# Performance work log

Measured on AMD Instinct MI355X. Metric: run time of the kernel, lower is better.

The kernel has to match this reference:

```python
import jax, jax.numpy as jnp
import numpy as np

B, S, T = 4, 512, 512
D, F, L, H, V = 512, 2048, 6, 8, 32000
HD = D // H


def setup_inputs() -> dict:
    key = jax.random.key(0)
    ks = list(jax.random.split(key, 16))
    it = iter(ks)

    def w(shape, scale=0.02):
        return jax.random.normal(next(it), shape, jnp.float32) * scale

    enc_in = jax.random.randint(next(it), (B, S), 0, V, dtype=jnp.int32)
    dec_in = jax.random.randint(next(it), (B, T), 0, V, dtype=jnp.int32)

    # sinusoidal positional encoding (make_sine_pos_encoding)
    pos = np.arange(S)[:, None].astype(np.float32)
    i = np.arange(D)[None, :].astype(np.float32)
    angle = pos / np.power(10000.0, (2.0 * np.floor(i / 2.0)) / D)
    pe = np.zeros((S, D), np.float32)
    pe[:, 0::2] = np.sin(angle[:, 0::2])
    pe[:, 1::2] = np.cos(angle[:, 1::2])

    return {
        "enc_in": enc_in,
        "dec_in": dec_in,
        "e_embed": w((V, D)),
        "d_embed": w((V, D)),
        "pos_enc": jnp.asarray(pe),
        "enc_mha_W": w((L, 4, D, D)),      # q,k,v,out
        "enc_mha_b": jnp.zeros((L, 4, D), jnp.float32),
        "enc_ln_g": jnp.ones((L, 2, D), jnp.float32),
        "enc_ln_b": jnp.zeros((L, 2, D), jnp.float32),
        "enc_ffn_W1": w((L, D, F)),
        "enc_ffn_b1": jnp.zeros((L, F), jnp.float32),
        "enc_ffn_W2": w((L, F, D)),
        "enc_ffn_b2": jnp.zeros((L, D), jnp.float32),
        "dec_mha_W": w((L, 8, D, D)),      # self q,k,v,out then cross q,k,v,out
        "dec_mha_b": jnp.zeros((L, 8, D), jnp.float32),
        "dec_ln_g": jnp.ones((L, 3, D), jnp.float32),
        "dec_ln_b": jnp.zeros((L, 3, D), jnp.float32),
        "dec_ffn_W1": w((L, D, F)),
        "dec_ffn_b1": jnp.zeros((L, F), jnp.float32),
        "dec_ffn_W2": w((L, F, D)),
        "dec_ffn_b2": jnp.zeros((L, D), jnp.float32),
    }


def _layer_norm(x, g, b, eps=1e-6):
    m = jnp.mean(x, axis=-1, keepdims=True)
    v = jnp.mean(jnp.square(x - m), axis=-1, keepdims=True)
    return (x - m) * jax.lax.rsqrt(v + eps) * g + b


def _split_heads(x):
    b, n, _ = x.shape
    return x.reshape(b, n, H, HD).transpose(0, 2, 1, 3)  # b h n d


def _mha(xq, xkv, W, b, mask):
    # W: [>=4, D, D] slice of (q,k,v,out); mask: broadcastable to [b,h,nq,nk]
    q = _split_heads(xq @ W[0] + b[0])
    k = _split_heads(xkv @ W[1] + b[1])
    v = _split_heads(xkv @ W[2] + b[2])
    s = jnp.einsum('bhqd,bhkd->bhqk', q, k) / jnp.sqrt(jnp.float32(HD))
    s = s + mask * (-1e9)
    a = jax.nn.softmax(s, axis=-1)
    o = jnp.einsum('bhqk,bhkd->bhqd', a, v)
    o = o.transpose(0, 2, 1, 3).reshape(xq.shape[0], xq.shape[1], D)
    return o @ W[3] + b[3]


def _forward(enc_in, dec_in, e_embed, d_embed, pos_enc,
             enc_mha_W, enc_mha_b, enc_ln_g, enc_ln_b,
             enc_ffn_W1, enc_ffn_b1, enc_ffn_W2, enc_ffn_b2,
             dec_mha_W, dec_mha_b, dec_ln_g, dec_ln_b,
             dec_ffn_W1, dec_ffn_b1, dec_ffn_W2, dec_ffn_b2):
    # masks: 1.0 where attention is blocked
    enc_pad = (enc_in == 0).astype(jnp.float32)[:, None, None, :]   # [B,1,1,S]
    dec_pad = (dec_in == 0).astype(jnp.float32)[:, None, None, :]   # [B,1,1,T]
    la = jnp.triu(jnp.ones((T, T), jnp.float32), k=1)[None, None]   # [1,1,T,T]
    look_ahead = jnp.maximum(la, dec_pad)                           # [B,1,T,T]

    scale = jnp.float32(D) ** 0.5
    e = e_embed[enc_in] * scale + pos_enc[None, :S]
    d = d_embed[dec_in] * scale + pos_enc[None, :T]

    for l in range(L):
        y = _mha(e, e, enc_mha_W[l], enc_mha_b[l], enc_pad)
        e = _layer_norm(e + y, enc_ln_g[l, 0], enc_ln_b[l, 0])
        y = jax.nn.relu(e @ enc_ffn_W1[l] + enc_ffn_b1[l]) @ enc_ffn_W2[l] + enc_ffn_b2[l]
        e = _layer_norm(e + y, enc_ln_g[l, 1], enc_ln_b[l, 1])

    for l in range(L):
        y = _mha(d, d, dec_mha_W[l, 0:4], dec_mha_b[l, 0:4], look_ahead)
        d = _layer_norm(d + y, dec_ln_g[l, 0], dec_ln_b[l, 0])
        y = _mha(d, e, dec_mha_W[l, 4:8], dec_mha_b[l, 4:8], enc_pad)
        d = _layer_norm(d + y, dec_ln_g[l, 1], dec_ln_b[l, 1])
        y = jax.nn.relu(d @ dec_ffn_W1[l] + dec_ffn_b1[l]) @ dec_ffn_W2[l] + dec_ffn_b2[l]
        d = _layer_norm(d + y, dec_ln_g[l, 2], dec_ln_b[l, 2])

    return d @ d_embed.T  # [B,T,V] logits


def reference(enc_in, dec_in, e_embed, d_embed, pos_enc,
              enc_mha_W, enc_mha_b, enc_ln_g, enc_ln_b,
              enc_ffn_W1, enc_ffn_b1, enc_ffn_W2, enc_ffn_b2,
              dec_mha_W, dec_mha_b, dec_ln_g, dec_ln_b,
              dec_ffn_W1, dec_ffn_b1, dec_ffn_W2, dec_ffn_b2):
    return _forward(enc_in, dec_in, e_embed, d_embed, pos_enc,
                    enc_mha_W, enc_mha_b, enc_ln_g, enc_ln_b,
                    enc_ffn_W1, enc_ffn_b1, enc_ffn_W2, enc_ffn_b2,
                    dec_mha_W, dec_mha_b, dec_ln_g, dec_ln_b,
                    dec_ffn_W1, dec_ffn_b1, dec_ffn_W2, dec_ffn_b2)
```

## Files before the change

### kernel.cpp

```cpp
#include <hip/hip_runtime.h>
#include <hip/hip_bf16.h>
#include <math.h>

#define B_ 4
#define S_ 512
#define D_ 512
#define F_ 2048
#define L_ 6
#define H_ 8
#define V_ 32000

typedef unsigned short u16;
typedef __attribute__((ext_vector_type(8))) short bhalf8;
typedef __attribute__((ext_vector_type(4))) float f32x4;

__device__ __forceinline__ u16 f2b(float v) {
    unsigned x = __builtin_bit_cast(unsigned, v);
    return (u16)((x + 0x7FFFu + ((x >> 16) & 1u)) >> 16);
}

#define GLD16(g, l) __builtin_amdgcn_global_load_lds( \
    (const __attribute__((address_space(1))) void*)(g), \
    (__attribute__((address_space(3))) void*)(l), 16, 0, 0)

__device__ __forceinline__ float redmax16(float v) {
    #pragma unroll
    for (int m = 1; m < 16; m <<= 1) v = fmaxf(v, __shfl_xor(v, m));
    return v;
}
__device__ __forceinline__ float redsum16(float v) {
    #pragma unroll
    for (int m = 1; m < 16; m <<= 1) v += __shfl_xor(v, m);
    return v;
}

template<int NWR, int NWC, int WM, int WN, int OUT, int RELU, int MLOOP,
         int SPLITA, int NT, int VTT, int SWZ>
__global__ __launch_bounds__(NWR * NWC * 64)
void mfma_gemm(const u16* __restrict__ A, const u16* __restrict__ A2, int acut,
               const u16* __restrict__ B,
               const float* __restrict__ bias, void* __restrict__ Cv,
               int K, int lda, int ldb, int ldc,
               u16* __restrict__ vtp, int vc0, long zoffC)
{
    constexpr int BM = NWR * WM, BN = NWC * WN;
    constexpr int NW = NWR * NWC;
    constexpr int CH_A = BM / 16, CH_B = BN / 16, CH = CH_A + CH_B;
    constexpr int NI = WM / 16, NJ = WN / 16;
    constexpr int TSTR = BM + 8;

    __shared__ u16 As[2][BM * 32];
    __shared__ u16 Bs[2][BN * 32];
    __shared__ u16 TT[VTT ? 64 * TSTR : 8];

    const int tid = threadIdx.x;
    const int wid = tid >> 6, lane = tid & 63;
    const int wrow = wid / NWC, wcol = wid % NWC;
    long bn, bmbase;
    if (SWZ) {
        long b0 = blockIdx.x;
        long per = (long)gridDim.x >> 3;
        long w = (b0 & 7) * per + (b0 >> 3);
        constexpr int MB = 16 / MLOOP;
        bn = (w / MB) * BN;
        bmbase = w % MB;
    } else {
        bn = (long)blockIdx.x * BN;
        bmbase = (long)blockIdx.y;
    }
    const int r4 = lane >> 2, c4 = lane & 3;
    const int l15 = lane & 15, l4 = lane >> 4;

    const u16* Ause = (SPLITA && bn >= acut) ? A2 : A;
    const long kz = (long)blockIdx.z * K;
    Ause += kz;
    B += kz;

    #pragma unroll 1
    for (int mi = 0; mi < MLOOP; ++mi) {
        const long bm = (bmbase * MLOOP + mi) * BM;

        f32x4 acc[NI][NJ];
        #pragma unroll
        for (int i = 0; i < NI; ++i)
            #pragma unroll
            for (int j = 0; j < NJ; ++j)
                acc[i][j] = (f32x4){0.f, 0.f, 0.f, 0.f};

        #pragma unroll
        for (int t = 0; t < CH / NW; ++t) {
            int c = wid + t * NW;
            if (c < CH_A) {
                GLD16(Ause + (bm + c * 16 + r4) * (long)lda + c4 * 8,
                      &As[0][c * 512 + lane * 8]);
            } else {
                int cb = c - CH_A;
                GLD16(B + (bn + cb * 16 + r4) * (long)ldb + c4 * 8,
                      &Bs[0][cb * 512 + lane * 8]);
            }
        }

        for (int k0 = 0; k0 < K; k0 += 32) {
            const int cur = (k0 >> 5) & 1;
            __syncthreads();
            if (k0 + 32 < K) {
                const int kn = k0 + 32;
                #pragma unroll
                for (int t = 0; t < CH / NW; ++t) {
                    int c = wid + t * NW;
                    if (c < CH_A) {
                        GLD16(Ause + (bm + c * 16 + r4) * (long)lda + kn + c4 * 8,
                              &As[cur ^ 1][c * 512 + lane * 8]);
                    } else {
                        int cb = c - CH_A;
                        GLD16(B + (bn + cb * 16 + r4) * (long)ldb + kn + c4 * 8,
                              &Bs[cur ^ 1][cb * 512 + lane * 8]);
                    }
                }
            }
            bhalf8 af[NI], bfr[NJ];
            #pragma unroll
            for (int i = 0; i < NI; ++i)
                af[i] = *(const bhalf8*)&As[cur][(wrow * WM + i * 16 + l15) * 32 + l4 * 8];
            #pragma unroll
            for (int j = 0; j < NJ; ++j)
                bfr[j] = *(const bhalf8*)&Bs[cur][(wcol * WN + j * 16 + l15) * 32 + l4 * 8];
            #pragma unroll
            for (int i = 0; i < NI; ++i)
                #pragma unroll
                for (int j = 0; j < NJ; ++j)
                    acc[i][j] = __builtin_amdgcn_mfma_f32_16x16x32_bf16(af[i], bfr[j], acc[i][j], 0, 0, 0);
        }

        if (VTT && vtp != nullptr && bn >= vc0) {
            #pragma unroll
            for (int j = 0; j < NJ; ++j) {
                const int cc = wcol * WN + j * 16 + l15;
                const float bv = bias ? bias[bn + cc] : 0.f;
                #pragma unroll
                for (int i = 0; i < NI; ++i) {
                    const int rw = wrow * WM + i * 16 + (l4 << 2);
                    #pragma unroll
                    for (int r = 0; r < 4; ++r)
                        TT[cc * TSTR + rw + r] = f2b(acc[i][j][r] + bv);
                }
            }
            __syncthreads();
            {
                const int cc = tid;
                const u16* src = &TT[cc * TSTR];
                u16* dst = &vtp[(bn - vc0 + cc) * 2048 + bm];
                #pragma unroll
                for (int p = 0; p < BM / 8; ++p)
                    *(uint4*)(dst + p * 8) = *(const uint4*)(src + p * 8);
            }
            __syncthreads();
            continue;
        }

        float* Cf = (float*)Cv + blockIdx.z * zoffC;
        u16*   Cb = (u16*)Cv  + blockIdx.z * zoffC;
        const int rowb = wrow * WM + (l4 << 2);
        const int colb = wcol * WN + l15;
        #pragma unroll
        for (int j = 0; j < NJ; ++j) {
            const long gc = bn + colb + j * 16;
            const float bv = bias ? bias[gc] : 0.f;
            #pragma unroll
            for (int i = 0; i < NI; ++i) {
                const long gr = bm + rowb + i * 16;
                #pragma unroll
                for (int r = 0; r < 4; ++r) {
                    float v = acc[i][j][r] + bv;
                    if (RELU) v = fmaxf(v, 0.f);
                    if (OUT == 0) {
                        if (NT) __builtin_nontemporal_store(v, &Cf[(gr + r) * (long)ldc + gc]);
                        else    Cf[(gr + r) * (long)ldc + gc] = v;
                    } else {
                        Cb[(gr + r) * (long)ldc + gc] = f2b(v);
                    }
                }
            }
        }
    }
}

__global__ __launch_bounds__(512)
void gemm_ln_kernel(const u16* __restrict__ A, const u16* __restrict__ B,
                    const float* __restrict__ bias,
                    float* __restrict__ x, u16* __restrict__ xb,
                    const float* __restrict__ g, const float* __restrict__ bb,
                    int K)
{
    __shared__ u16 As[16 * 32];
    __shared__ u16 Bs[512 * 32];
    __shared__ float red[2][16][8];
    __shared__ float mv[2][16];

    const int tid = threadIdx.x, w = tid >> 6, lane = tid & 63;
    const int l15 = lane & 15, l4 = lane >> 4;
    const int r4 = lane >> 2, c4 = lane & 3;
    const long bm = (long)blockIdx.x * 16;

    f32x4 acc[4];
    #pragma unroll
    for (int j = 0; j < 4; ++j) acc[j] = (f32x4){0.f, 0.f, 0.f, 0.f};

    for (int k0 = 0; k0 < K; k0 += 32) {
        #pragma unroll
        for (int t = 0; t < 5; ++t) {
            int c = w + t * 8;
            if (c < 33) {
                if (c == 0) {
                    GLD16(A + (bm + r4) * (long)K + k0 + c4 * 8, As + lane * 8);
                } else {
                    GLD16(B + ((c - 1) * 16 + r4) * (long)K + k0 + c4 * 8,
                          Bs + (c - 1) * 512 + lane * 8);
                }
            }
        }
        __syncthreads();
        bhalf8 af = *(const bhalf8*)&As[l15 * 32 + l4 * 8];
        #pragma unroll
        for (int j = 0; j < 4; ++j) {
            bhalf8 bf = *(const bhalf8*)&Bs[(w * 64 + j * 16 + l15) * 32 + l4 * 8];
            acc[j] = __builtin_amdgcn_mfma_f32_16x16x32_bf16(af, bf, acc[j], 0, 0, 0);
        }
        __syncthreads();
    }

    float vbuf[4][4], s[4] = {0, 0, 0, 0}, s2[4] = {0, 0, 0, 0};
    #pragma unroll
    for (int j = 0; j < 4; ++j) {
        int col = w * 64 + j * 16 + l15;
        float bv = bias[col];
        #pragma unroll
        for (int r = 0; r < 4; ++r) {
            int row = l4 * 4 + r;
            float v = acc[j][r] + bv + x[(bm + row) * 512 + col];
            vbuf[j][r] = v;
            s[r] += v; s2[r] += v * v;
        }
    }
    #pragma unroll
    for (int r = 0; r < 4; ++r) { s[r] = redsum16(s[r]); s2[r] = redsum16(s2[r]); }
    if (l15 == 0) {
        #pragma unroll
        for (int r = 0; r < 4; ++r) {
            red[0][l4 * 4 + r][w] = s[r];
            red[1][l4 * 4 + r][w] = s2[r];
        }
    }
    __syncthreads();
    if (tid < 16) {
        float S = 0.f, S2 = 0.f;
        #pragma unroll
        for (int q = 0; q < 8; ++q) { S += red[0][tid][q]; S2 += red[1][tid][q]; }
        float mean = S * (1.f / 512.f);
        float var = S2 * (1.f / 512.f) - mean * mean;
        mv[0][tid] = mean;
        mv[1][tid] = rsqrtf(var + 1e-6f);
    }
    __syncthreads();
    #pragma unroll
    for (int j = 0; j < 4; ++j) {
        int col = w * 64 + j * 16 + l15;
        float gg = g[col], bbv = bb[col];
        #pragma unroll
        for (int r = 0; r < 4; ++r) {
            int row = l4 * 4 + r;
            float o = (vbuf[j][r] - mv[0][row]) * mv[1][row] * gg + bbv;
            x[(bm + row) * 512 + col] = o;
            xb[(bm + row) * 512 + col] = f2b(o);
        }
    }
}

template<int CAUSAL>
__global__ __launch_bounds__(256)
void flash_kernel(const u16* __restrict__ Qp, int ldq,
                  const u16* __restrict__ Kp, int ldk,
                  const u16* __restrict__ Vt,
                  const int* __restrict__ tok,
                  u16* __restrict__ Op)
{
    __shared__ u16 QS[64 * 64];
    __shared__ u16 KS[2][64 * 64];
    __shared__ u16 VS[2][64 * 64];
    __shared__ u16 PS[4 * 16 * 64];
    __shared__ float MK[512];

    const int tid = threadIdx.x, lane = tid & 63, w = tid >> 6;
    const int l15 = lane & 15, l4 = lane >> 4;
    const int qb = blockIdx.x, bh = blockIdx.y;
    const int b = bh >> 3, h = bh & 7;

    const u16* Q = Qp + (long)(b * 512 + qb * 64) * ldq + h * 64;
    const u16* K = Kp + (long)(b * 512) * ldk + h * 64;
    const u16* V = Vt + (long)(h * 64) * 2048 + b * 512;
    u16* O = Op + (long)(b * 512 + qb * 64) * 512 + h * 64;

    {
        int t0 = tok[b * 512 + tid];
        int t1 = tok[b * 512 + 256 + tid];
        MK[tid]       = (t0 == 0) ? -1e9f : 0.f;
        MK[tid + 256] = (t1 == 0) ? -1e9f : 0.f;
    }
    const int r = tid >> 3;
    const int c = (tid & 7) ^ (r & 7);
    {
        GLD16(Q + (long)r * ldq + c * 8,        QS + tid * 8);
        GLD16(Q + (long)(r + 32) * ldq + c * 8, QS + 2048 + tid * 8);
        GLD16(K + (long)r * ldk + c * 8,              KS[0] + tid * 8);
        GLD16(K + (long)(32 + r) * ldk + c * 8,       KS[0] + 2048 + tid * 8);
        GLD16(V + (long)r * 2048 + c * 8,             VS[0] + tid * 8);
        GLD16(V + (long)(r + 32) * 2048 + c * 8,      VS[0] + 2048 + tid * 8);
    }
    __syncthreads();

    bhalf8 qa[2];
    #pragma unroll
    for (int kc = 0; kc < 2; ++kc) {
        int row = w * 16 + l15;
        qa[kc] = *(const bhalf8*)&QS[row * 64 + (((kc * 4 + l4) ^ (row & 7)) << 3)];
    }

    f32x4 oacc[4];
    float mrun[4], lrun[4];
    #pragma unroll
    for (int j = 0; j < 4; ++j) oacc[j] = (f32x4){0.f, 0.f, 0.f, 0.f};
    #pragma unroll
    for (int rr = 0; rr < 4; ++rr) { mrun[rr] = -1e30f; lrun[rr] = 0.f; }

    const int tmax = CAUSAL ? qb : 7;

    for (int t = 0; t <= tmax; ++t) {
        const int cur = t & 1;
        if (t < tmax) {
            const int tn = t + 1;
            GLD16(K + (long)(tn * 64 + r) * ldk + c * 8,        KS[cur ^ 1] + tid * 8);
            GLD16(K + (long)(tn * 64 + 32 + r) * ldk + c * 8,   KS[cur ^ 1] + 2048 + tid * 8);
            GLD16(V + (long)r * 2048 + tn * 64 + c * 8,         VS[cur ^ 1] + tid * 8);
            GLD16(V + (long)(r + 32) * 2048 + tn * 64 + c * 8,  VS[cur ^ 1] + 2048 + tid * 8);
        }
        f32x4 sac[4];
        #pragma unroll
        for (int jj = 0; jj < 4; ++jj) sac[jj] = (f32x4){0.f, 0.f, 0.f, 0.f};
        bhalf8 kf[4][2];
        #pragma unroll
        for (int jj = 0; jj < 4; ++jj)
            #pragma unroll
            for (int kc = 0; kc < 2; ++kc) {
                int row = jj * 16 + l15;
                kf[jj][kc] = *(const bhalf8*)&KS[cur][row * 64 + (((kc * 4 + l4) ^ (row & 7)) << 3)];
            }
        #pragma unroll
        for (int jj = 0; jj < 4; ++jj)
            #pragma unroll
            for (int kc = 0; kc < 2; ++kc)
                sac[jj] = __builtin_amdgcn_mfma_f32_16x16x32_bf16(qa[kc], kf[jj][kc], sac[jj], 0, 0, 0);

        #pragma unroll
        for (int jj = 0; jj < 4; ++jj) {
            float mk = MK[t * 64 + jj * 16 + l15];
            #pragma unroll
            for (int rr = 0; rr < 4; ++rr) {
                float mk2 = mk;
                if (CAUSAL && t == qb) {
                    int col = t * 64 + jj * 16 + l15;
                    int qr = qb * 64 + w * 16 + l4 * 4 + rr;
                    if (col > qr) mk2 = -1e9f;
                }
                sac[jj][rr] = sac[jj][rr] * 0.125f + mk2;
            }
        }
        #pragma unroll
        for (int rr = 0; rr < 4; ++rr) {
            float mx = fmaxf(fmaxf(sac[0][rr], sac[1][rr]), fmaxf(sac[2][rr], sac[3][rr]));
            mx = redmax16(mx);
            float mnew = fmaxf(mrun[rr], mx);
            float alpha = __expf(mrun[rr] - mnew);
            float sum = 0.f;
            int row_p = l4 * 4 + rr;
            #pragma unroll
            for (int jj = 0; jj < 4; ++jj) {
                float pv = __expf(sac[jj][rr] - mnew);
                sum += pv;
                int kv = jj * 16 + l15;
                PS[w * 1024 + row_p * 64 + ((((kv >> 3) ^ (row_p & 7)) << 3) | (kv & 7))] = f2b(pv);
            }
            sum = redsum16(sum);
            lrun[rr] = lrun[rr] * alpha + sum;
            mrun[rr] = mnew;
            #pragma unroll
            for (int jd = 0; jd < 4; ++jd) oacc[jd][rr] *= alpha;
        }
        bhalf8 pa[2], vf[4][2];
        #pragma unroll
        for (int kc = 0; kc < 2; ++kc) {
            int row = l15;
            pa[kc] = *(const bhalf8*)&PS[w * 1024 + row * 64 + (((kc * 4 + l4) ^ (row & 7)) << 3)];
        }
        #pragma unroll
        for (int jd = 0; jd < 4; ++jd)
            #pragma unroll
            for (int kc = 0; kc < 2; ++kc) {
                int row = jd * 16 + l15;
                vf[jd][kc] = *(const bhalf8*)&VS[cur][row * 64 + (((kc * 4 + l4) ^ (row & 7)) << 3)];
            }
        #pragma unroll
        for (int jd = 0; jd < 4; ++jd)
            #pragma unroll
            for (int kc = 0; kc < 2; ++kc)
                oacc[jd] = __builtin_amdgcn_mfma_f32_16x16x32_bf16(pa[kc], vf[jd][kc], oacc[jd], 0, 0, 0);
        __syncthreads();
    }

    #pragma unroll
    for (int rr = 0; rr < 4; ++rr) {
        float inv = 1.f / lrun[rr];
        int row = w * 16 + l4 * 4 + rr;
        #pragma unroll
        for (int jd = 0; jd < 4; ++jd)
            O[(long)row * 512 + jd * 16 + l15] = f2b(oacc[jd][rr] * inv);
    }
}

__global__ __launch_bounds__(256)
void transpose_many(const float* __restrict__ inA, const float* __restrict__ inB,
                    int zsplit, int R, int C, u16* __restrict__ out)
{
    int z = blockIdx.z;
    const float* in = (z < zsplit) ? inA + (long)z * R * C
                                   : inB + (long)(z - zsplit) * R * C;
    u16* o = out + (long)z * R * C;
    __shared__ float tb[64][65];
    const int tr = blockIdx.y * 64, tc = blockIdx.x * 64;
    const int col = threadIdx.x & 63, r0 = threadIdx.x >> 6;
    #pragma unroll
    for (int p = 0; p < 16; ++p) {
        int row = r0 * 16 + p;
        tb[row][col] = in[(long)(tr + row) * C + tc + col];
    }
    __syncthreads();
    #pragma unroll
    for (int p = 0; p < 16; ++p) {
        int row = r0 * 16 + p;
        o[(long)(tc + row) * R + tr + col] = f2b(tb[col][row]);
    }
}

__global__ __launch_bounds__(256)
void convert_b16(const float4* __restrict__ in, u16* __restrict__ out, long n4)
{
    long i = (long)blockIdx.x * 256 + threadIdx.x;
    if (i >= n4) return;
    float4 v = in[i];
    uint2 p;
    p.x = (unsigned)f2b(v.x) | ((unsigned)f2b(v.y) << 16);
    p.y = (unsigned)f2b(v.z) | ((unsigned)f2b(v.w) << 16);
    *(uint2*)(out + i * 4) = p;
}

__global__ __launch_bounds__(256)
void embed_kernel(const int* __restrict__ tE, const int* __restrict__ tD,
                  const float* __restrict__ eE, const float* __restrict__ eD,
                  const float* __restrict__ pos,
                  float* __restrict__ xE, float* __restrict__ xD,
                  u16* __restrict__ bE, u16* __restrict__ bD, float scale)
{
    const int z = blockIdx.y;
    const int* tok = z ? tD : tE;
    const float* emb = z ? eD : eE;
    float* x = z ? xD : xE;
    u16* xb = z ? bD : bE;
    int row = blockIdx.x;
    int s = row & (S_ - 1);
    int t = tok[row];
    const float* er = emb + (long)t * D_;
    const float* pr = pos + (long)s * D_;
    float* o = x + (long)row * D_;
    u16*  ob = xb + (long)row * D_;
    int i = threadIdx.x;
    float v0 = er[i]       * scale + pr[i];
    float v1 = er[i + 256] * scale + pr[i + 256];
    o[i] = v0;        o[i + 256] = v1;
    ob[i] = f2b(v0);  ob[i + 256] = f2b(v1);
}

__global__ __launch_bounds__(256)
void add_ln_kernel(float* __restrict__ x, const float* __restrict__ y0,
                   const float* __restrict__ y1, const float* __restrict__ cb,
                   u16* __restrict__ xb,
                   const float* __restrict__ g, const float* __restrict__ bb)
{
    long row = blockIdx.x;
    float* xr = x + row * D_;
    u16* xo = xb + row * D_;
    const float* yr0 = y0 + row * D_;
    const float* yr1 = y1 + row * D_;
    int t = threadIdx.x, t2 = t + 256;

    float r0 = xr[t]  + yr0[t]  + yr1[t]  + cb[t];
    float r1 = xr[t2] + yr0[t2] + yr1[t2] + cb[t2];
    float s = r0 + r1;
    float s2 = r0 * r0 + r1 * r1;
    #pragma unroll
    for (int i = 1; i < 64; i <<= 1) {
        s  += __shfl_xor(s, i);
        s2 += __shfl_xor(s2, i);
    }
    __shared__ float rs[4], rs2[4];
    int wid = t >> 6;
    if ((t & 63) == 0) { rs[wid] = s; rs2[wid] = s2; }
    __syncthreads();
    s  = rs[0] + rs[1] + rs[2] + rs[3];
    s2 = rs2[0] + rs2[1] + rs2[2] + rs2[3];

    float mean = s * (1.f / D_);
    float var  = s2 * (1.f / D_) - mean * mean;
    float inv  = rsqrtf(var + 1e-6f);
    float o0 = (r0 - mean) * inv * g[t]  + bb[t];
    float o1 = (r1 - mean) * inv * g[t2] + bb[t2];
    xr[t] = o0;       xr[t2] = o1;
    xo[t] = f2b(o0);  xo[t2] = f2b(o1);
}

extern "C" void kernel_launch(void* const* d_in, const int* in_sizes, int n_in,
                              void* d_out, int out_size, void* d_ws, size_t ws_size,
                              hipStream_t stream)
{
    const int*   enc_in     = (const int*)  d_in[0];
    const int*   dec_in     = (const int*)  d_in[1];
    const float* e_embed    = (const float*)d_in[2];
    const float* d_embed    = (const float*)d_in[3];
    const float* pos_enc    = (const float*)d_in[4];
    const float* enc_mha_W  = (const float*)d_in[5];
    const float* enc_mha_b  = (const float*)d_in[6];
    const float* enc_ln_g   = (const float*)d_in[7];
    const float* enc_ln_b   = (const float*)d_in[8];
    const float* enc_ffn_W1 = (const float*)d_in[9];
    const float* enc_ffn_b1 = (const float*)d_in[10];
    const float* enc_ffn_W2 = (const float*)d_in[11];
    const float* enc_ffn_b2 = (const float*)d_in[12];
    const float* dec_mha_W  = (const float*)d_in[13];
    const float* dec_mha_b  = (const float*)d_in[14];
    const float* dec_ln_g   = (const float*)d_in[15];
    const float* dec_ln_b   = (const float*)d_in[16];
    const float* dec_ffn_W1 = (const float*)d_in[17];
    const float* dec_ffn_b1 = (const float*)d_in[18];
    const float* dec_ffn_W2 = (const float*)d_in[19];
    const float* dec_ffn_b2 = (const float*)d_in[20];
    float* out = (float*)d_out;

    const int  BS  = B_ * S_;
    const long BSD = (long)BS * D_;
    const long DD  = (long)D_ * D_;
    const long DF  = (long)D_ * F_;

    char* p = (char*)d_ws;
    auto alloc = [&](long bytes) { char* r = p; p += (bytes + 255) & ~255L; return r; };
    float* e    = (float*)alloc(BSD * 4);
    float* dd   = (float*)alloc(BSD * 4);
    float* y    = (float*)alloc(2 * BSD * 4);
    u16*   eb   = (u16*)  alloc(BSD * 2);
    u16*   ddb  = (u16*)  alloc(BSD * 2);
    u16*   qkv  = (u16*)  alloc((long)BS * 1536 * 2);
    u16*   att  = (u16*)  alloc(BSD * 2);
    u16*   vt   = (u16*)  alloc(BSD * 2);
    u16*   ffnh = (u16*)  alloc((long)BS * F_ * 2);
    u16*   wEmb = (u16*)  alloc((long)V_ * D_ * 2);
    u16*   wMha = (u16*)  alloc(72 * DD * 2);
    u16*   wF1  = (u16*)  alloc(12 * DF * 2);
    u16*   wF2  = (u16*)  alloc(12 * DF * 2);

    transpose_many<<<dim3(8, 8, 72), 256, 0, stream>>>(enc_mha_W, dec_mha_W, 24, 512, 512, wMha);
    transpose_many<<<dim3(32, 8, 12), 256, 0, stream>>>(enc_ffn_W1, dec_ffn_W1, 6, 512, 2048, wF1);
    transpose_many<<<dim3(8, 32, 12), 256, 0, stream>>>(enc_ffn_W2, dec_ffn_W2, 6, 2048, 512, wF2);
    convert_b16<<<16000, 256, 0, stream>>>((const float4*)d_embed, wEmb, (long)V_ * D_ / 4);

    const float scale = sqrtf((float)D_);
    embed_kernel<<<dim3(BS, 2), 256, 0, stream>>>(enc_in, dec_in, e_embed, d_embed,
                                                  pos_enc, e, dd, eb, ddb, scale);

    #define GEMM_SKV(A, Bp, bias, C) \
        mfma_gemm<1,1,32,64,1,0,1,0,0,1,0><<<dim3(24, 64), 64, 0, stream>>>( \
            A, A, 1 << 30, Bp, bias, C, 512, 512, 512, 1536, vt, 1024, 0)
    #define GEMM_FFN1(A, Bp, bias, C) \
        mfma_gemm<2,2,64,64,1,1,1,0,0,0,0><<<dim3(16, 16), 256, 0, stream>>>( \
            A, A, 1 << 30, Bp, bias, C, 512, 512, 512, 2048, nullptr, 0, 0)
    #define GEMM_FFN2(A, Bp) \
        mfma_gemm<2,1,32,64,0,0,1,0,0,0,0><<<dim3(8, 32, 2), 128, 0, stream>>>( \
            A, A, 1 << 30, Bp, nullptr, y, 1024, 2048, 2048, 512, nullptr, 0, BSD)

    for (int l = 0; l < L_; ++l) {
        const u16* Wl = wMha + (long)l * 4 * DD;
        const float* bl = enc_mha_b + (long)l * 4 * D_;
        GEMM_SKV(eb, Wl, bl, qkv);
        flash_kernel<0><<<dim3(8, 32), 256, 0, stream>>>(qkv, 1536, qkv + 512, 1536, vt, enc_in, att);
        gemm_ln_kernel<<<128, 512, 0, stream>>>(att, Wl + 3 * DD, bl + 3 * D_,
            e, eb, enc_ln_g + (long)(l * 2) * D_, enc_ln_b + (long)(l * 2) * D_, 512);
        GEMM_FFN1(eb, wF1 + (long)l * DF, enc_ffn_b1 + (long)l * F_, ffnh);
        GEMM_FFN2(ffnh, wF2 + (long)l * DF);
        add_ln_kernel<<<BS, 256, 0, stream>>>(e, y, y + BSD, enc_ffn_b2 + (long)l * D_, eb,
            enc_ln_g + (long)(l * 2 + 1) * D_, enc_ln_b + (long)(l * 2 + 1) * D_);
    }

    for (int l = 0; l < L_; ++l) {
        const u16* Wl = wMha + (long)(24 + l * 8) * DD;
        const float* bl = dec_mha_b + (long)l * 8 * D_;
        GEMM_SKV(ddb, Wl, bl, qkv);
        flash_kernel<1><<<dim3(8, 32), 256, 0, stream>>>(qkv, 1536, qkv + 512, 1536, vt, dec_in, att);
        gemm_ln_kernel<<<128, 512, 0, stream>>>(att, Wl + 3 * DD, bl + 3 * D_,
            dd, ddb, dec_ln_g + (long)(l * 3) * D_, dec_ln_b + (long)(l * 3) * D_, 512);
        mfma_gemm<1,1,32,64,1,0,1,1,0,1,0><<<dim3(24, 64), 64, 0, stream>>>(
            ddb, eb, 512, Wl + 4 * DD, bl + 4 * D_, qkv,
            512, 512, 512, 1536, vt, 1024, 0);
        flash_kernel<0><<<dim3(8, 32), 256, 0, stream>>>(qkv, 1536, qkv + 512, 1536, vt, enc_in, att);
        gemm_ln_kernel<<<128, 512, 0, stream>>>(att, Wl + 7 * DD, bl + 7 * D_,
            dd, ddb, dec_ln_g + (long)(l * 3 + 1) * D_, dec_ln_b + (long)(l * 3 + 1) * D_, 512);
        GEMM_FFN1(ddb, wF1 + (long)(6 + l) * DF, dec_ffn_b1 + (long)l * F_, ffnh);
        GEMM_FFN2(ffnh, wF2 + (long)(6 + l) * DF);
        add_ln_kernel<<<BS, 256, 0, stream>>>(dd, y, y + BSD, dec_ffn_b2 + (long)l * D_, ddb,
            dec_ln_g + (long)(l * 3 + 2) * D_, dec_ln_b + (long)(l * 3 + 2) * D_);
    }

    mfma_gemm<2,2,64,64,0,0,2,0,1,0,1><<<dim3(2000), 256, 0, stream>>>(
        ddb, ddb, 1 << 30, wEmb, nullptr, out, 512, 512, 512, 32000, nullptr, 0, 0);
}
```

Baseline: 1.689 ms.

## Fuse FFN up-projection, ReLU, down-projection, residual and LayerNorm into one kernel

Replaces the FFN1 GEMM, the split-K FFN2 GEMM and the add+LayerNorm kernel with a single ffn_kernel. Each block handles 16 rows: it keeps the hidden activations in shared memory (XOR-swizzled), computes the 512-to-2048 and 2048-to-512 projections with bf16 MFMA, then applies bias, residual and LayerNorm in registers. This removes two launches per layer and the global round-trips of the hidden and partial-output buffers. In exchange, only 128 blocks run, and every block streams the full W1 and W2 weights from global memory/L2 with little reuse, which may make it bandwidth- or latency-bound.

```diff
diff --git a/kernel.cpp b/kernel.cpp
--- a/kernel.cpp
+++ b/kernel.cpp
@@ -41,7 +41,7 @@
                const u16* __restrict__ B,
                const float* __restrict__ bias, void* __restrict__ Cv,
                int K, int lda, int ldb, int ldc,
-               u16* __restrict__ vtp, int vc0, long zoffC)
+               u16* __restrict__ vtp, int vc0)
 {
     constexpr int BM = NWR * WM, BN = NWC * WN;
     constexpr int NW = NWR * NWC;
@@ -72,9 +72,6 @@
     const int l15 = lane & 15, l4 = lane >> 4;
 
     const u16* Ause = (SPLITA && bn >= acut) ? A2 : A;
-    const long kz = (long)blockIdx.z * K;
-    Ause += kz;
-    B += kz;
 
     #pragma unroll 1
     for (int mi = 0; mi < MLOOP; ++mi) {
@@ -158,8 +155,8 @@
             continue;
         }
 
-        float* Cf = (float*)Cv + blockIdx.z * zoffC;
-        u16*   Cb = (u16*)Cv  + blockIdx.z * zoffC;
+        float* Cf = (float*)Cv;
+        u16*   Cb = (u16*)Cv;
         const int rowb = wrow * WM + (l4 << 2);
         const int colb = wcol * WN + l15;
         #pragma unroll
@@ -238,6 +235,117 @@
         for (int r = 0; r < 4; ++r) {
             int row = l4 * 4 + r;
             float v = acc[j][r] + bv + x[(bm + row) * 512 + col];
+            vbuf[j][r] = v;
+            s[r] += v; s2[r] += v * v;
+        }
+    }
+    #pragma unroll
+    for (int r = 0; r < 4; ++r) { s[r] = redsum16(s[r]); s2[r] = redsum16(s2[r]); }
+    if (l15 == 0) {
+        #pragma unroll
+        for (int r = 0; r < 4; ++r) {
+            red[0][l4 * 4 + r][w] = s[r];
+            red[1][l4 * 4 + r][w] = s2[r];
+        }
+    }
+    __syncthreads();
+    if (tid < 16) {
+        float S = 0.f, S2 = 0.f;
+        #pragma unroll
+        for (int q = 0; q < 8; ++q) { S += red[0][tid][q]; S2 += red[1][tid][q]; }
+        float mean = S * (1.f / 512.f);
+        float var = S2 * (1.f / 512.f) - mean * mean;
+        mv[0][tid] = mean;
+        mv[1][tid] = rsqrtf(var + 1e-6f);
+    }
+    __syncthreads();
+    #pragma unroll
+    for (int j = 0; j < 4; ++j) {
+        int col = w * 64 + j * 16 + l15;
+        float gg = g[col], bbv = bb[col];
+        #pragma unroll
+        for (int r = 0; r < 4; ++r) {
+            int row = l4 * 4 + r;
+            float o = (vbuf[j][r] - mv[0][row]) * mv[1][row] * gg + bbv;
+            x[(bm + row) * 512 + col] = o;
+            xb[(bm + row) * 512 + col] = f2b(o);
+        }
+    }
+}
+
+__global__ __launch_bounds__(512)
+void ffn_kernel(const u16* __restrict__ Axb, const u16* __restrict__ W1,
+                const float* __restrict__ b1, const u16* __restrict__ W2,
+                const float* __restrict__ b2,
+                float* __restrict__ x, u16* __restrict__ xb,
+                const float* __restrict__ g, const float* __restrict__ bb)
+{
+    __shared__ u16 As[16 * 512];
+    __shared__ u16 Hs[16 * 2048];
+    __shared__ float red[2][16][8];
+    __shared__ float mv[2][16];
+
+    const int tid = threadIdx.x, w = tid >> 6, lane = tid & 63;
+    const int l15 = lane & 15, l4 = lane >> 4;
+    const long bm = (long)blockIdx.x * 16;
+
+    {
+        int r0 = w, r1 = w + 8;
+        GLD16(Axb + (bm + r0) * 512 + ((lane ^ (r0 & 7)) << 3), As + r0 * 512 + lane * 8);
+        GLD16(Axb + (bm + r1) * 512 + ((lane ^ (r1 & 7)) << 3), As + r1 * 512 + lane * 8);
+    }
+    __syncthreads();
+
+    #pragma unroll
+    for (int nt = 0; nt < 4; ++nt) {
+        const int nbase = w * 256 + nt * 64;
+        f32x4 acc[4];
+        #pragma unroll
+        for (int j = 0; j < 4; ++j) acc[j] = (f32x4){0.f, 0.f, 0.f, 0.f};
+        #pragma unroll
+        for (int ks = 0; ks < 16; ++ks) {
+            bhalf8 af = *(const bhalf8*)&As[l15 * 512 + (((ks * 4 + l4) ^ (l15 & 7)) << 3)];
+            #pragma unroll
+            for (int j = 0; j < 4; ++j) {
+                bhalf8 bf = *(const bhalf8*)&W1[(long)(nbase + j * 16 + l15) * 512 + ks * 32 + l4 * 8];
+                acc[j] = __builtin_amdgcn_mfma_f32_16x16x32_bf16(af, bf, acc[j], 0, 0, 0);
+            }
+        }
+        #pragma unroll
+        for (int j = 0; j < 4; ++j) {
+            int coln = nbase + j * 16 + l15;
+            float bv = b1[coln];
+            #pragma unroll
+            for (int r = 0; r < 4; ++r) {
+                int row = l4 * 4 + r;
+                float v = fmaxf(acc[j][r] + bv, 0.f);
+                Hs[row * 2048 + ((((coln >> 3) ^ (row & 7)) << 3) | (coln & 7))] = f2b(v);
+            }
+        }
+    }
+    __syncthreads();
+
+    f32x4 acc2[4];
+    #pragma unroll
+    for (int j = 0; j < 4; ++j) acc2[j] = (f32x4){0.f, 0.f, 0.f, 0.f};
+    for (int ks = 0; ks < 64; ++ks) {
+        bhalf8 af = *(const bhalf8*)&Hs[l15 * 2048 + (((ks * 4 + l4) ^ (l15 & 7)) << 3)];
+        #pragma unroll
+        for (int j = 0; j < 4; ++j) {
+            bhalf8 bf = *(const bhalf8*)&W2[(long)(w * 64 + j * 16 + l15) * 2048 + ks * 32 + l4 * 8];
+            acc2[j] = __builtin_amdgcn_mfma_f32_16x16x32_bf16(af, bf, acc2[j], 0, 0, 0);
+        }
+    }
+
+    float vbuf[4][4], s[4] = {0, 0, 0, 0}, s2[4] = {0, 0, 0, 0};
+    #pragma unroll
+    for (int j = 0; j < 4; ++j) {
+        int col = w * 64 + j * 16 + l15;
+        float bv = b2[col];
+        #pragma unroll
+        for (int r = 0; r < 4; ++r) {
+            int row = l4 * 4 + r;
+            float v = acc2[j][r] + bv + x[(bm + row) * 512 + col];
             vbuf[j][r] = v;
             s[r] += v; s2[r] += v * v;
         }
@@ -486,44 +594,6 @@
     float v1 = er[i + 256] * scale + pr[i + 256];
     o[i] = v0;        o[i + 256] = v1;
     ob[i] = f2b(v0);  ob[i + 256] = f2b(v1);
-}
-
-__global__ __launch_bounds__(256)
-void add_ln_kernel(float* __restrict__ x, const float* __restrict__ y0,
-                   const float* __restrict__ y1, const float* __restrict__ cb,
-                   u16* __restrict__ xb,
-                   const float* __restrict__ g, const float* __restrict__ bb)
-{
-    long row = blockIdx.x;
-    float* xr = x + row * D_;
-    u16* xo = xb + row * D_;
-    const float* yr0 = y0 + row * D_;
-    const float* yr1 = y1 + row * D_;
-    int t = threadIdx.x, t2 = t + 256;
-
-    float r0 = xr[t]  + yr0[t]  + yr1[t]  + cb[t];
-    float r1 = xr[t2] + yr0[t2] + yr1[t2] + cb[t2];
-    float s = r0 + r1;
-    float s2 = r0 * r0 + r1 * r1;
-    #pragma unroll
-    for (int i = 1; i < 64; i <<= 1) {
-        s  += __shfl_xor(s, i);
-        s2 += __shfl_xor(s2, i);
-    }
-    __shared__ float rs[4], rs2[4];
-    int wid = t >> 6;
-    if ((t & 63) == 0) { rs[wid] = s; rs2[wid] = s2; }
-    __syncthreads();
-    s  = rs[0] + rs[1] + rs[2] + rs[3];
-    s2 = rs2[0] + rs2[1] + rs2[2] + rs2[3];
-
-    float mean = s * (1.f / D_);
-    float var  = s2 * (1.f / D_) - mean * mean;
-    float inv  = rsqrtf(var + 1e-6f);
-    float o0 = (r0 - mean) * inv * g[t]  + bb[t];
-    float o1 = (r1 - mean) * inv * g[t2] + bb[t2];
-    xr[t] = o0;       xr[t2] = o1;
-    xo[t] = f2b(o0);  xo[t2] = f2b(o1);
 }
 
 extern "C" void kernel_launch(void* const* d_in, const int* in_sizes, int n_in,
@@ -562,13 +632,11 @@
     auto alloc = [&](long bytes) { char* r = p; p += (bytes + 255) & ~255L; return r; };
     float* e    = (float*)alloc(BSD * 4);
     float* dd   = (float*)alloc(BSD * 4);
-    float* y    = (float*)alloc(2 * BSD * 4);
     u16*   eb   = (u16*)  alloc(BSD * 2);
     u16*   ddb  = (u16*)  alloc(BSD * 2);
     u16*   qkv  = (u16*)  alloc((long)BS * 1536 * 2);
     u16*   att  = (u16*)  alloc(BSD * 2);
     u16*   vt   = (u16*)  alloc(BSD * 2);
-    u16*   ffnh = (u16*)  alloc((long)BS * F_ * 2);
     u16*   wEmb = (u16*)  alloc((long)V_ * D_ * 2);
     u16*   wMha = (u16*)  alloc(72 * DD * 2);
     u16*   wF1  = (u16*)  alloc(12 * DF * 2);
@@ -585,13 +653,7 @@
 
     #define GEMM_SKV(A, Bp, bias, C) \
         mfma_gemm<1,1,32,64,1,0,1,0,0,1,0><<<dim3(24, 64), 64, 0, stream>>>( \
-            A, A, 1 << 30, Bp, bias, C, 512, 512, 512, 1536, vt, 1024, 0)
-    #define GEMM_FFN1(A, Bp, bias, C) \
-        mfma_gemm<2,2,64,64,1,1,1,0,0,0,0><<<dim3(16, 16), 256, 0, stream>>>( \
-            A, A, 1 << 30, Bp, bias, C, 512, 512, 512, 2048, nullptr, 0, 0)
-    #define GEMM_FFN2(A, Bp) \
-        mfma_gemm<2,1,32,64,0,0,1,0,0,0,0><<<dim3(8, 32, 2), 128, 0, stream>>>( \
-            A, A, 1 << 30, Bp, nullptr, y, 1024, 2048, 2048, 512, nullptr, 0, BSD)
+            A, A, 1 << 30, Bp, bias, C, 512, 512, 512, 1536, vt, 1024)
 
     for (int l = 0; l < L_; ++l) {
         const u16* Wl = wMha + (long)l * 4 * DD;
@@ -600,10 +662,9 @@
         flash_kernel<0><<<dim3(8, 32), 256, 0, stream>>>(qkv, 1536, qkv + 512, 1536, vt, enc_in, att);
         gemm_ln_kernel<<<128, 512, 0, stream>>>(att, Wl + 3 * DD, bl + 3 * D_,
             e, eb, enc_ln_g + (long)(l * 2) * D_, enc_ln_b + (long)(l * 2) * D_, 512);
-        GEMM_FFN1(eb, wF1 + (long)l * DF, enc_ffn_b1 + (long)l * F_, ffnh);
-        GEMM_FFN2(ffnh, wF2 + (long)l * DF);
-        add_ln_kernel<<<BS, 256, 0, stream>>>(e, y, y + BSD, enc_ffn_b2 + (long)l * D_, eb,
-            enc_ln_g + (long)(l * 2 + 1) * D_, enc_ln_b + (long)(l * 2 + 1) * D_);
+        ffn_kernel<<<128, 512, 0, stream>>>(eb, wF1 + (long)l * DF, enc_ffn_b1 + (long)l * F_,
+            wF2 + (long)l * DF, enc_ffn_b2 + (long)l * D_,
+            e, eb, enc_ln_g + (long)(l * 2 + 1) * D_, enc_ln_b + (long)(l * 2 + 1) * D_);
     }
 
     for (int l = 0; l < L_; ++l) {
@@ -615,16 +676,15 @@
             dd, ddb, dec_ln_g + (long)(l * 3) * D_, dec_ln_b + (long)(l * 3) * D_, 512);
         mfma_gemm<1,1,32,64,1,0,1,1,0,1,0><<<dim3(24, 64), 64, 0, stream>>>(
             ddb, eb, 512, Wl + 4 * DD, bl + 4 * D_, qkv,
-            512, 512, 512, 1536, vt, 1024, 0);
+            512, 512, 512, 1536, vt, 1024);
         flash_kernel<0><<<dim3(8, 32), 256, 0, stream>>>(qkv, 1536, qkv + 512, 1536, vt, enc_in, att);
         gemm_ln_kernel<<<128, 512, 0, stream>>>(att, Wl + 7 * DD, bl + 7 * D_,
             dd, ddb, dec_ln_g + (long)(l * 3 + 1) * D_, dec_ln_b + (long)(l * 3 + 1) * D_, 512);
-        GEMM_FFN1(ddb, wF1 + (long)(6 + l) * DF, dec_ffn_b1 + (long)l * F_, ffnh);
-        GEMM_FFN2(ffnh, wF2 + (long)(6 + l) * DF);
-        add_ln_kernel<<<BS, 256, 0, stream>>>(dd, y, y + BSD, dec_ffn_b2 + (long)l * D_, ddb,
-            dec_ln_g + (long)(l * 3 + 2) * D_, dec_ln_b + (long)(l * 3 + 2) * D_);
+        ffn_kernel<<<128, 512, 0, stream>>>(ddb, wF1 + (long)(6 + l) * DF, dec_ffn_b1 + (long)l * F_,
+            wF2 + (long)(6 + l) * DF, dec_ffn_b2 + (long)l * D_,
+            dd, ddb, dec_ln_g + (long)(l * 3 + 2) * D_, dec_ln_b + (long)(l * 3 + 2) * D_);
     }
 
     mfma_gemm<2,2,64,64,0,0,2,0,1,0,1><<<dim3(2000), 256, 0, stream>>>(
-        ddb, ddb, 1 << 30, wEmb, nullptr, out, 512, 512, 512, 32000, nullptr, 0, 0);
-}
+        ddb, ddb, 1 << 30, wEmb, nullptr, out, 512, 512, 512, 32000, nullptr, 0);
+}
```

Result: slower. 2.539 ms (+50.3%).
